# Kernel tuning notes

Hardware: AMD Instinct MI355X
Metric: run time of the kernel (lower is better)

Reference implementation:

```python
import jax, jax.numpy as jnp
import numpy as np

B, C, G, E, R, T, L, K = 8, 192, 256, 384, 4, 8192, 3, 3
DILATIONS = (1, 3, 9)
EPS = 1e-5


def setup_inputs() -> dict:
    key = jax.random.key(0)
    ks = jax.random.split(key, 16)
    s = 0.05
    return {
        'x': jax.random.normal(ks[0], (B, C, T), jnp.float32),
        'x_mask': jnp.ones((B, 1, T), jnp.float32),
        'g': jax.random.normal(ks[1], (B, G, 1), jnp.float32),
        'dconv_w': jax.random.normal(ks[2], (L, C, K), jnp.float32) * s,
        'dconv_b': jax.random.normal(ks[3], (L, C), jnp.float32) * s,
        'ln_gamma': jnp.ones((L, C), jnp.float32),
        'ln_beta': jnp.zeros((L, C), jnp.float32),
        'p1_w': jax.random.normal(ks[4], (L, E, C), jnp.float32) * s,
        'p1_b': jax.random.normal(ks[5], (L, E), jnp.float32) * s,
        'p1_ain_w': jax.random.normal(ks[6], (L, C * R, G), jnp.float32) * 0.01,
        'p1_ain_b': jnp.zeros((L, C * R), jnp.float32),
        'p1_aout_w': jax.random.normal(ks[7], (L, E * R, G), jnp.float32) * 0.01,
        'p1_aout_b': jnp.zeros((L, E * R), jnp.float32),
        'p2_w': jax.random.normal(ks[8], (L, C, E), jnp.float32) * s,
        'p2_b': jax.random.normal(ks[9], (L, C), jnp.float32) * s,
        'p2_ain_w': jax.random.normal(ks[10], (L, E * R, G), jnp.float32) * 0.01,
        'p2_ain_b': jnp.zeros((L, E * R), jnp.float32),
        'p2_aout_w': jax.random.normal(ks[11], (L, C * R, G), jnp.float32) * 0.01,
        'p2_aout_b': jnp.zeros((L, C * R), jnp.float32),
    }


def _causal_dconv(x, w, b, dilation):
    # x: [B,C,T]; w: [C,K] depthwise kernel; matches flip/pad/conv/flip in torch module
    xf = jnp.flip(x, 2)
    xf = jnp.pad(xf, ((0, 0), (0, 0), (0, (K - 1) * dilation)))
    y = jax.lax.conv_general_dilated(
        xf, w[:, None, :], window_strides=(1,), padding='VALID',
        rhs_dilation=(dilation,), dimension_numbers=('NCH', 'OIH', 'NCH'),
        feature_group_count=C)
    y = y + b[None, :, None]
    return jnp.flip(y, 2)


def _layernorm_c(x, gamma, beta):
    # LayerNorm over channel axis (axis=1)
    mu = jnp.mean(x, axis=1, keepdims=True)
    var = jnp.mean(jnp.square(x - mu), axis=1, keepdims=True)
    xn = (x - mu) * jax.lax.rsqrt(var + EPS)
    return xn * gamma[None, :, None] + beta[None, :, None]


def _lora(x, g2, w_main, b_main, ain_w, ain_b, aout_w, aout_b, cin, cout):
    # main 1x1 conv
    x_ = jnp.einsum('oc,bcl->bol', w_main, x) + b_main[None, :, None]
    a_in = (g2 @ ain_w.T + ain_b).reshape(-1, cin, R)      # [B,cin,R]
    a_out = (g2 @ aout_w.T + aout_b).reshape(-1, R, cout)  # [B,R,cout]
    t = jnp.einsum('bcl,bcr->brl', x, a_in)
    low = jnp.einsum('brl,brc->bcl', t, a_out)
    return x_ + low


def reference(x, x_mask, g, dconv_w, dconv_b, ln_gamma, ln_beta,
              p1_w, p1_b, p1_ain_w, p1_ain_b, p1_aout_w, p1_aout_b,
              p2_w, p2_b, p2_ain_w, p2_ain_b, p2_aout_w, p2_aout_b):
    g2 = g[:, :, 0]  # [B,G]
    x = x * x_mask
    for i in range(L):
        residual = x
        h = _causal_dconv(x, dconv_w[i], dconv_b[i], DILATIONS[i])
        h = _layernorm_c(h, ln_gamma[i], ln_beta[i])
        h = h * x_mask
        h = _lora(h, g2, p1_w[i], p1_b[i], p1_ain_w[i], p1_ain_b[i],
                  p1_aout_w[i], p1_aout_b[i], C, E)
        h = jax.nn.gelu(h, approximate=False)
        h = _lora(h, g2, p2_w[i], p2_b[i], p2_ain_w[i], p2_ain_b[i],
                  p2_aout_w[i], p2_aout_b[i], E, C)
        x = residual + h
    return x
```

## Files before the change

kernel.cpp:

```cpp
#include <hip/hip_runtime.h>
#include <hip/hip_bf16.h>

#define B_ 8
#define C_ 192
#define G_ 256
#define E_ 384
#define R_ 4
#define T_ 8192
#define L_ 3
#define K_ 3

typedef __attribute__((ext_vector_type(4))) float f32x4;
typedef __attribute__((ext_vector_type(8))) short bf16x8;
typedef __attribute__((ext_vector_type(4))) short bf16x4;

static __device__ __forceinline__ float bf2f(short u) {
    union { float f; unsigned int i; } z;
    z.i = ((unsigned int)(unsigned short)u) << 16;
    return z.f;
}

static __device__ __forceinline__ float gelu_fast(float x) {
    float e = __expf(-1.702f * x);
    return x / (1.0f + e);
}

__global__ __launch_bounds__(256) void adapters_kernel(
    const float* __restrict__ g2,
    const float* __restrict__ w0, const float* __restrict__ bi0, float* __restrict__ o0,
    const float* __restrict__ w1, const float* __restrict__ bi1, float* __restrict__ o1,
    const float* __restrict__ w2, const float* __restrict__ bi2, float* __restrict__ o2,
    const float* __restrict__ w3, const float* __restrict__ bi3, float* __restrict__ o3)
{
    const int N0 = L_ * B_ * (C_ * R_);
    const int N1 = L_ * B_ * (E_ * R_);
    int idx = blockIdx.x * 256 + threadIdx.x;
    const float* w; const float* bi; float* o; int rows; int li;
    if (idx < N0)                      { w=w0; bi=bi0; o=o0; rows=C_*R_; li=idx; }
    else if ((idx -= N0) < N1)         { w=w1; bi=bi1; o=o1; rows=E_*R_; li=idx; }
    else if ((idx -= N1) < N1)         { w=w2; bi=bi2; o=o2; rows=E_*R_; li=idx; }
    else if ((idx -= N1) < N0)         { w=w3; bi=bi3; o=o3; rows=C_*R_; li=idx; }
    else return;
    int bb = li & 7;
    int lr = li >> 3;
    const float4* wr = (const float4*)(w + (size_t)lr * G_);
    const float4* gb = (const float4*)(g2 + (size_t)bb * G_);
    float s = bi[lr];
#pragma unroll 8
    for (int g = 0; g < G_ / 4; ++g) {
        float4 a = gb[g], b = wr[g];
        s = fmaf(a.x, b.x, s); s = fmaf(a.y, b.y, s);
        s = fmaf(a.z, b.z, s); s = fmaf(a.w, b.w, s);
    }
    o[((size_t)(lr / rows) * B_ + bb) * rows + (lr % rows)] = s;
}

__global__ __launch_bounds__(256) void builds_kernel(
    const float* __restrict__ p1w, const float* __restrict__ p2w,
    const float* __restrict__ gam, const float* __restrict__ bet,
    const float* __restrict__ A1in, const float* __restrict__ A1out,
    const float* __restrict__ A2in, const float* __restrict__ A2out,
    __hip_bfloat16* __restrict__ W1, __hip_bfloat16* __restrict__ W2,
    float* __restrict__ C1)
{
    const int W1B = (L_ * B_ * E_ * C_) / 256;
    int blk = blockIdx.x;
    if (blk < W1B) {
        int idx = blk * 256 + threadIdx.x;
        int c = idx % C_;
        int e = (idx / C_) % E_;
        int b = (idx / (C_ * E_)) % B_;
        int l = idx / (C_ * E_ * B_);
        float v = p1w[((size_t)l * E_ + e) * C_ + c];
        const float* ai = A1in + ((size_t)l * B_ + b) * (C_ * R_);
        const float* ao = A1out + ((size_t)l * B_ + b) * (R_ * E_);
#pragma unroll
        for (int r = 0; r < R_; ++r) v = fmaf(ai[c * R_ + r], ao[r * E_ + e], v);
        W1[idx] = __float2bfloat16(v * gam[l * C_ + c]);
    } else if (blk < 2 * W1B) {
        int idx = (blk - W1B) * 256 + threadIdx.x;
        int e = idx % E_;
        int c = (idx / E_) % C_;
        int b = (idx / (C_ * E_)) % B_;
        int l = idx / (C_ * E_ * B_);
        float v = p2w[((size_t)l * C_ + c) * E_ + e];
        const float* ai = A2in + ((size_t)l * B_ + b) * (E_ * R_);
        const float* ao = A2out + ((size_t)l * B_ + b) * (R_ * C_);
#pragma unroll
        for (int r = 0; r < R_; ++r) v = fmaf(ai[e * R_ + r], ao[r * C_ + c], v);
        W2[idx] = __float2bfloat16(v);
    } else {
        int idx = (blk - 2 * W1B) * 256 + threadIdx.x;
        if (idx >= L_ * B_ * E_) return;
        int e = idx % E_;
        int b = (idx / E_) % B_;
        int l = idx / (E_ * B_);
        const float* wrow = p1w + ((size_t)l * E_ + e) * C_;
        const float* ai = A1in + ((size_t)l * B_ + b) * (C_ * R_);
        const float* ao = A1out + ((size_t)l * B_ + b) * (R_ * E_);
        const float* bt = bet + l * C_;
        float s = 0.f;
        for (int c = 0; c < C_; ++c) {
            float v = wrow[c];
#pragma unroll
            for (int r = 0; r < R_; ++r) v = fmaf(ai[c * R_ + r], ao[r * E_ + e], v);
            s = fmaf(v, bt[c], s);
        }
        C1[((size_t)l * B_ + b) * E_ + e] = s;
    }
}

__global__ __launch_bounds__(256) void transpose_in_kernel(
    const float* __restrict__ x, const float* __restrict__ mask,
    __hip_bfloat16* __restrict__ xw)
{
    __shared__ float tile[64][65];
    int b = blockIdx.z, c0 = blockIdx.y * 64, t0 = blockIdx.x * 64;
#pragma unroll
    for (int it = 0; it < 4; ++it) {
        int i = it * 256 + threadIdx.x;
        int r = i >> 4, cq = i & 15;
        float4 xv = *(const float4*)(&x[((size_t)b * C_ + c0 + r) * T_ + t0 + cq * 4]);
        float4 mv = *(const float4*)(&mask[(size_t)b * T_ + t0 + cq * 4]);
        tile[r][cq * 4 + 0] = xv.x * mv.x;
        tile[r][cq * 4 + 1] = xv.y * mv.y;
        tile[r][cq * 4 + 2] = xv.z * mv.z;
        tile[r][cq * 4 + 3] = xv.w * mv.w;
    }
    __syncthreads();
#pragma unroll
    for (int it = 0; it < 4; ++it) {
        int i = it * 256 + threadIdx.x;
        int r = i >> 4, cq = i & 15;
        union { __hip_bfloat16 h[4]; int2 i2; } u;
#pragma unroll
        for (int j = 0; j < 4; ++j) u.h[j] = __float2bfloat16(tile[cq * 4 + j][r]);
        *(int2*)(&xw[((size_t)b * T_ + t0 + r) * C_ + c0 + cq * 4]) = u.i2;
    }
}

__global__ __launch_bounds__(256) void transpose_out_kernel(
    const __hip_bfloat16* __restrict__ xw, float* __restrict__ out)
{
    __shared__ float tile[64][65];
    int b = blockIdx.z, c0 = blockIdx.y * 64, t0 = blockIdx.x * 64;
#pragma unroll
    for (int it = 0; it < 4; ++it) {
        int i = it * 256 + threadIdx.x;
        int r = i >> 4, cq = i & 15;
        bf16x4 v = *(const bf16x4*)(&xw[((size_t)b * T_ + t0 + r) * C_ + c0 + cq * 4]);
#pragma unroll
        for (int j = 0; j < 4; ++j) tile[cq * 4 + j][r] = bf2f(v[j]);
    }
    __syncthreads();
#pragma unroll
    for (int it = 0; it < 4; ++it) {
        int i = it * 256 + threadIdx.x;
        int r = i >> 4, cq = i & 15;
        float4 o;
        o.x = tile[r][cq * 4 + 0];
        o.y = tile[r][cq * 4 + 1];
        o.z = tile[r][cq * 4 + 2];
        o.w = tile[r][cq * 4 + 3];
        *(float4*)(&out[((size_t)b * C_ + c0 + r) * T_ + t0 + cq * 4]) = o;
    }
}

__global__ __launch_bounds__(256, 2) void ffn_fused_kernel(
    const __hip_bfloat16* __restrict__ xin, __hip_bfloat16* __restrict__ xout,
    const float* __restrict__ dw, const float* __restrict__ db,
    const float* __restrict__ mask,
    const __hip_bfloat16* __restrict__ W1, const float* __restrict__ b1,
    const float* __restrict__ c1,
    const __hip_bfloat16* __restrict__ W2, const float* __restrict__ b2,
    int dil)
{
    __shared__ __hip_bfloat16 Hs[64][C_ + 8];
    __shared__ __hip_bfloat16 H1s[64][E_ + 8];
    const int b = blockIdx.y;
    const int t0 = blockIdx.x * 64;
    const int tid = threadIdx.x;
    const int wv = tid >> 6, lane = tid & 63;
    const int llo = lane & 15, lhi = lane >> 4;
    const size_t xbase = (size_t)b * T_ * C_;

    {
        const int grp = tid >> 4, gl = tid & 15;
        const int cbase = gl * 12;
        float4 wf[9], dbf[3];
#pragma unroll
        for (int q = 0; q < 9; ++q) wf[q] = *(const float4*)(dw + cbase * 3 + q * 4);
#pragma unroll
        for (int q = 0; q < 3; ++q) dbf[q] = *(const float4*)(db + cbase + q * 4);
#pragma unroll
        for (int rr = 0; rr < 4; ++rr) {
            int tl = grp * 4 + rr;
            int t = t0 + tl;
            float v[12];
#pragma unroll
            for (int j = 0; j < 12; ++j) v[j] = ((const float*)dbf)[j];
#pragma unroll
            for (int k3 = 0; k3 < 3; ++k3) {
                int tt = t - k3 * dil;
                if (tt >= 0) {
                    const __hip_bfloat16* rp = xin + xbase + (size_t)tt * C_ + cbase;
#pragma unroll
                    for (int q = 0; q < 3; ++q) {
                        bf16x4 xv = *(const bf16x4*)(rp + q * 4);
#pragma unroll
                        for (int jj = 0; jj < 4; ++jj) {
                            int j = q * 4 + jj;
                            v[j] = fmaf(((const float*)wf)[j * 3 + k3], bf2f(xv[jj]), v[j]);
                        }
                    }
                }
            }
            float s = 0.f, sq = 0.f;
#pragma unroll
            for (int j = 0; j < 12; ++j) { s += v[j]; sq = fmaf(v[j], v[j], sq); }
#pragma unroll
            for (int o = 1; o <= 8; o <<= 1) {
                s += __shfl_xor(s, o, 64);
                sq += __shfl_xor(sq, o, 64);
            }
            float mu = s * (1.f / C_);
            float var = fmaf(sq, 1.f / C_, -mu * mu);
            float rs = rsqrtf(var + 1e-5f);
            float m = mask[(size_t)b * T_ + t];
            float sc = rs * m;
            float sh = -mu * sc;
            union { __hip_bfloat16 h[12]; int2 i2[3]; } u;
#pragma unroll
            for (int j = 0; j < 12; ++j)
                u.h[j] = __float2bfloat16(fmaf(v[j], sc, sh));
#pragma unroll
            for (int q = 0; q < 3; ++q)
                *(int2*)(&Hs[tl][cbase + q * 4]) = u.i2[q];
        }
    }
    __syncthreads();

    const __hip_bfloat16* w1p = W1 + (size_t)b * E_ * C_
        + (size_t)(wv * 96 + llo) * C_ + lhi * 8;
    f32x4 acc1[6][4] = {};
    {
        bf16x8 af[6], afn[6], bfr[4], bfrn[4];
#pragma unroll
        for (int mf = 0; mf < 6; ++mf)
            af[mf] = *(const bf16x8*)(w1p + (size_t)mf * 16 * C_);
#pragma unroll
        for (int nf = 0; nf < 4; ++nf)
            bfr[nf] = *(const bf16x8*)(&Hs[nf * 16 + llo][lhi * 8]);
#pragma unroll
        for (int kc = 0; kc < 6; ++kc) {
            if (kc < 5) {
#pragma unroll
                for (int mf = 0; mf < 6; ++mf)
                    afn[mf] = *(const bf16x8*)(w1p + (size_t)mf * 16 * C_ + (kc + 1) * 32);
#pragma unroll
                for (int nf = 0; nf < 4; ++nf)
                    bfrn[nf] = *(const bf16x8*)(&Hs[nf * 16 + llo][(kc + 1) * 32 + lhi * 8]);
            }
#pragma unroll
            for (int mf = 0; mf < 6; ++mf)
#pragma unroll
                for (int nf = 0; nf < 4; ++nf)
                    acc1[mf][nf] = __builtin_amdgcn_mfma_f32_16x16x32_bf16(
                        af[mf], bfr[nf], acc1[mf][nf], 0, 0, 0);
#pragma unroll
            for (int mf = 0; mf < 6; ++mf) af[mf] = afn[mf];
#pragma unroll
            for (int nf = 0; nf < 4; ++nf) bfr[nf] = bfrn[nf];
        }
    }

    float mcol[4];
#pragma unroll
    for (int nf = 0; nf < 4; ++nf)
        mcol[nf] = mask[(size_t)b * T_ + t0 + nf * 16 + llo];
#pragma unroll
    for (int mf = 0; mf < 6; ++mf) {
        int e0 = wv * 96 + mf * 16 + lhi * 4;
        float4 b1v = *(const float4*)(b1 + e0);
        float4 c1v = *(const float4*)(c1 + (size_t)b * E_ + e0);
#pragma unroll
        for (int nf = 0; nf < 4; ++nf) {
            union { __hip_bfloat16 h[4]; int2 i2; } u;
#pragma unroll
            for (int j = 0; j < 4; ++j) {
                float xx = acc1[mf][nf][j] + ((const float*)&b1v)[j]
                         + mcol[nf] * ((const float*)&c1v)[j];
                u.h[j] = __float2bfloat16(gelu_fast(xx));
            }
            *(int2*)(&H1s[nf * 16 + llo][e0]) = u.i2;
        }
    }
    __syncthreads();

    const __hip_bfloat16* w2p = W2 + (size_t)b * C_ * E_
        + (size_t)(wv * 48 + llo) * E_ + lhi * 8;
    f32x4 acc2[3][4] = {};
    {
        bf16x8 af[3], afn[3], bfr[4], bfrn[4];
#pragma unroll
        for (int mf = 0; mf < 3; ++mf)
            af[mf] = *(const bf16x8*)(w2p + (size_t)mf * 16 * E_);
#pragma unroll
        for (int nf = 0; nf < 4; ++nf)
            bfr[nf] = *(const bf16x8*)(&H1s[nf * 16 + llo][lhi * 8]);
#pragma unroll
        for (int kc = 0; kc < 12; ++kc) {
            if (kc < 11) {
#pragma unroll
                for (int mf = 0; mf < 3; ++mf)
                    afn[mf] = *(const bf16x8*)(w2p + (size_t)mf * 16 * E_ + (kc + 1) * 32);
#pragma unroll
                for (int nf = 0; nf < 4; ++nf)
                    bfrn[nf] = *(const bf16x8*)(&H1s[nf * 16 + llo][(kc + 1) * 32 + lhi * 8]);
            }
#pragma unroll
            for (int mf = 0; mf < 3; ++mf)
#pragma unroll
                for (int nf = 0; nf < 4; ++nf)
                    acc2[mf][nf] = __builtin_amdgcn_mfma_f32_16x16x32_bf16(
                        af[mf], bfr[nf], acc2[mf][nf], 0, 0, 0);
#pragma unroll
            for (int mf = 0; mf < 3; ++mf) af[mf] = afn[mf];
#pragma unroll
            for (int nf = 0; nf < 4; ++nf) bfr[nf] = bfrn[nf];
        }
    }

#pragma unroll
    for (int mf = 0; mf < 3; ++mf) {
        int c0 = wv * 48 + mf * 16 + lhi * 4;
        float4 b2v = *(const float4*)(b2 + c0);
#pragma unroll
        for (int nf = 0; nf < 4; ++nf) {
            int t = t0 + nf * 16 + llo;
            const __hip_bfloat16* pr = xin + xbase + (size_t)t * C_ + c0;
            __hip_bfloat16* po = xout + xbase + (size_t)t * C_ + c0;
            union { __hip_bfloat16 h[4]; int2 i2; } ui, uo;
            ui.i2 = *(const int2*)pr;
#pragma unroll
            for (int j = 0; j < 4; ++j)
                uo.h[j] = __float2bfloat16(
                    bf2f(*(short*)&ui.h[j]) + acc2[mf][nf][j] + ((const float*)&b2v)[j]);
            *(int2*)po = uo.i2;
        }
    }
}

extern "C" void kernel_launch(void* const* d_in, const int* in_sizes, int n_in,
                              void* d_out, int out_size, void* d_ws, size_t ws_size,
                              hipStream_t stream) {
    const float* x        = (const float*)d_in[0];
    const float* x_mask   = (const float*)d_in[1];
    const float* g        = (const float*)d_in[2];
    const float* dconv_w  = (const float*)d_in[3];
    const float* dconv_b  = (const float*)d_in[4];
    const float* ln_gamma = (const float*)d_in[5];
    const float* ln_beta  = (const float*)d_in[6];
    const float* p1_w     = (const float*)d_in[7];
    const float* p1_b     = (const float*)d_in[8];
    const float* p1_ain_w = (const float*)d_in[9];
    const float* p1_ain_b = (const float*)d_in[10];
    const float* p1_aout_w= (const float*)d_in[11];
    const float* p1_aout_b= (const float*)d_in[12];
    const float* p2_w     = (const float*)d_in[13];
    const float* p2_b     = (const float*)d_in[14];
    const float* p2_ain_w = (const float*)d_in[15];
    const float* p2_ain_b = (const float*)d_in[16];
    const float* p2_aout_w= (const float*)d_in[17];
    const float* p2_aout_b= (const float*)d_in[18];

    char* ws = (char*)d_ws;
    size_t off = 0;
    __hip_bfloat16* xwA = (__hip_bfloat16*)(ws + off); off += (size_t)B_ * T_ * C_ * 2;
    __hip_bfloat16* xwB = (__hip_bfloat16*)(ws + off); off += (size_t)B_ * T_ * C_ * 2;
    __hip_bfloat16* W1 = (__hip_bfloat16*)(ws + off);  off += (size_t)L_ * B_ * E_ * C_ * 2;
    __hip_bfloat16* W2 = (__hip_bfloat16*)(ws + off);  off += (size_t)L_ * B_ * C_ * E_ * 2;
    float* C1    = (float*)(ws + off); off += (size_t)L_ * B_ * E_ * 4;
    float* A1in  = (float*)(ws + off); off += (size_t)L_ * B_ * C_ * R_ * 4;
    float* A1out = (float*)(ws + off); off += (size_t)L_ * B_ * R_ * E_ * 4;
    float* A2in  = (float*)(ws + off); off += (size_t)L_ * B_ * E_ * R_ * 4;
    float* A2out = (float*)(ws + off); off += (size_t)L_ * B_ * R_ * C_ * 4;

    {
        int total = L_ * B_ * (2 * C_ * R_ + 2 * E_ * R_);
        adapters_kernel<<<(total + 255) / 256, 256, 0, stream>>>(
            g,
            p1_ain_w, p1_ain_b, A1in,
            p1_aout_w, p1_aout_b, A1out,
            p2_ain_w, p2_ain_b, A2in,
            p2_aout_w, p2_aout_b, A2out);
    }
    {
        int w1blocks = (L_ * B_ * E_ * C_) / 256;
        int c1blocks = (L_ * B_ * E_ + 255) / 256;
        builds_kernel<<<2 * w1blocks + c1blocks, 256, 0, stream>>>(
            p1_w, p2_w, ln_gamma, ln_beta,
            A1in, A1out, A2in, A2out, W1, W2, C1);
    }

    transpose_in_kernel<<<dim3(T_ / 64, C_ / 64, B_), 256, 0, stream>>>(x, x_mask, xwA);

    const int DILS[3] = {1, 3, 9};
    __hip_bfloat16* bufs[2] = {xwA, xwB};
    for (int l = 0; l < L_; ++l) {
        ffn_fused_kernel<<<dim3(T_ / 64, B_), 256, 0, stream>>>(
            bufs[l & 1], bufs[(l & 1) ^ 1],
            dconv_w + l * C_ * K_, dconv_b + l * C_, x_mask,
            W1 + (size_t)l * B_ * E_ * C_, p1_b + l * E_,
            C1 + (size_t)l * B_ * E_,
            W2 + (size_t)l * B_ * C_ * E_, p2_b + l * C_, DILS[l]);
    }

    transpose_out_kernel<<<dim3(T_ / 64, C_ / 64, B_), 256, 0, stream>>>(xwB, (float*)d_out);
}
```

Measured before the change: 264.5 us.

## Split fused FFN into two kernels with global H1 in MFMA-fragment layout

```diff
diff --git a/kernel.cpp b/kernel.cpp
--- a/kernel.cpp
+++ b/kernel.cpp
@@ -21,8 +21,13 @@
 }
 
 static __device__ __forceinline__ float gelu_fast(float x) {
-    float e = __expf(-1.702f * x);
-    return x / (1.0f + e);
+    float x2 = x * x;
+    float inner = fmaf(0.044715f * x, x2, x);
+    float e = __expf(1.5957691216057308f * inner);
+    float r = 1.0f / (e + 1.0f);
+    float t = fmaf(-2.0f, r, 1.0f);
+    float s = 0.5f * x;
+    return fmaf(s, t, s);
 }
 
 __global__ __launch_bounds__(256) void adapters_kernel(
@@ -166,21 +171,19 @@
     }
 }
 
-__global__ __launch_bounds__(256, 2) void ffn_fused_kernel(
-    const __hip_bfloat16* __restrict__ xin, __hip_bfloat16* __restrict__ xout,
+
+__global__ __launch_bounds__(512, 2) void stage_gemm1_kernel(
+    const __hip_bfloat16* __restrict__ xin,
     const float* __restrict__ dw, const float* __restrict__ db,
     const float* __restrict__ mask,
     const __hip_bfloat16* __restrict__ W1, const float* __restrict__ b1,
-    const float* __restrict__ c1,
-    const __hip_bfloat16* __restrict__ W2, const float* __restrict__ b2,
-    int dil)
+    const float* __restrict__ c1, __hip_bfloat16* __restrict__ H1, int dil)
 {
     __shared__ __hip_bfloat16 Hs[64][C_ + 8];
-    __shared__ __hip_bfloat16 H1s[64][E_ + 8];
     const int b = blockIdx.y;
     const int t0 = blockIdx.x * 64;
     const int tid = threadIdx.x;
-    const int wv = tid >> 6, lane = tid & 63;
+    const int w = tid >> 6, lane = tid & 63;
     const int llo = lane & 15, lhi = lane >> 4;
     const size_t xbase = (size_t)b * T_ * C_;
 
@@ -193,8 +196,8 @@
 #pragma unroll
         for (int q = 0; q < 3; ++q) dbf[q] = *(const float4*)(db + cbase + q * 4);
 #pragma unroll
-        for (int rr = 0; rr < 4; ++rr) {
-            int tl = grp * 4 + rr;
+        for (int rr = 0; rr < 2; ++rr) {
+            int tl = grp * 2 + rr;
             int t = t0 + tl;
             float v[12];
 #pragma unroll
@@ -241,12 +244,12 @@
     __syncthreads();
 
     const __hip_bfloat16* w1p = W1 + (size_t)b * E_ * C_
-        + (size_t)(wv * 96 + llo) * C_ + lhi * 8;
-    f32x4 acc1[6][4] = {};
+        + (size_t)(w * 48 + llo) * C_ + lhi * 8;
+    f32x4 acc1[3][4] = {};
     {
-        bf16x8 af[6], afn[6], bfr[4], bfrn[4];
-#pragma unroll
-        for (int mf = 0; mf < 6; ++mf)
+        bf16x8 af[3], afn[3], bfr[4], bfrn[4];
+#pragma unroll
+        for (int mf = 0; mf < 3; ++mf)
             af[mf] = *(const bf16x8*)(w1p + (size_t)mf * 16 * C_);
 #pragma unroll
         for (int nf = 0; nf < 4; ++nf)
@@ -255,20 +258,20 @@
         for (int kc = 0; kc < 6; ++kc) {
             if (kc < 5) {
 #pragma unroll
-                for (int mf = 0; mf < 6; ++mf)
+                for (int mf = 0; mf < 3; ++mf)
                     afn[mf] = *(const bf16x8*)(w1p + (size_t)mf * 16 * C_ + (kc + 1) * 32);
 #pragma unroll
                 for (int nf = 0; nf < 4; ++nf)
                     bfrn[nf] = *(const bf16x8*)(&Hs[nf * 16 + llo][(kc + 1) * 32 + lhi * 8]);
             }
 #pragma unroll
-            for (int mf = 0; mf < 6; ++mf)
+            for (int mf = 0; mf < 3; ++mf)
 #pragma unroll
                 for (int nf = 0; nf < 4; ++nf)
                     acc1[mf][nf] = __builtin_amdgcn_mfma_f32_16x16x32_bf16(
                         af[mf], bfr[nf], acc1[mf][nf], 0, 0, 0);
 #pragma unroll
-            for (int mf = 0; mf < 6; ++mf) af[mf] = afn[mf];
+            for (int mf = 0; mf < 3; ++mf) af[mf] = afn[mf];
 #pragma unroll
             for (int nf = 0; nf < 4; ++nf) bfr[nf] = bfrn[nf];
         }
@@ -279,8 +282,10 @@
     for (int nf = 0; nf < 4; ++nf)
         mcol[nf] = mask[(size_t)b * T_ + t0 + nf * 16 + llo];
 #pragma unroll
-    for (int mf = 0; mf < 6; ++mf) {
-        int e0 = wv * 96 + mf * 16 + lhi * 4;
+    for (int mf = 0; mf < 3; ++mf) {
+        int e0 = w * 48 + mf * 16 + lhi * 4;
+        int be = e0 >> 3;
+        int el = e0 & 7;
         float4 b1v = *(const float4*)(b1 + e0);
         float4 c1v = *(const float4*)(c1 + (size_t)b * E_ + e0);
 #pragma unroll
@@ -292,10 +297,24 @@
                          + mcol[nf] * ((const float*)&c1v)[j];
                 u.h[j] = __float2bfloat16(gelu_fast(xx));
             }
-            *(int2*)(&H1s[nf * 16 + llo][e0]) = u.i2;
-        }
-    }
-    __syncthreads();
+            size_t bt = (size_t)(b * 512 + (t0 >> 4) + nf);
+            *(int2*)(&H1[bt * 6144 + be * 128 + llo * 8 + el]) = u.i2;
+        }
+    }
+}
+
+__global__ __launch_bounds__(256, 2) void gemm2_kernel(
+    const __hip_bfloat16* __restrict__ H1,
+    const __hip_bfloat16* __restrict__ W2, const float* __restrict__ b2,
+    const __hip_bfloat16* __restrict__ xin, __hip_bfloat16* __restrict__ xout)
+{
+    const int b = blockIdx.y;
+    const int t0 = blockIdx.x * 64;
+    const int tid = threadIdx.x;
+    const int wv = tid >> 6, lane = tid & 63;
+    const int llo = lane & 15, lhi = lane >> 4;
+    const size_t xbase = (size_t)b * T_ * C_;
+    const __hip_bfloat16* h1b = H1 + (size_t)(b * 512 + (t0 >> 4)) * 6144;
 
     const __hip_bfloat16* w2p = W2 + (size_t)b * C_ * E_
         + (size_t)(wv * 48 + llo) * E_ + lhi * 8;
@@ -307,7 +326,7 @@
             af[mf] = *(const bf16x8*)(w2p + (size_t)mf * 16 * E_);
 #pragma unroll
         for (int nf = 0; nf < 4; ++nf)
-            bfr[nf] = *(const bf16x8*)(&H1s[nf * 16 + llo][lhi * 8]);
+            bfr[nf] = *(const bf16x8*)(h1b + (size_t)nf * 6144 + lhi * 128 + llo * 8);
 #pragma unroll
         for (int kc = 0; kc < 12; ++kc) {
             if (kc < 11) {
@@ -316,7 +335,8 @@
                     afn[mf] = *(const bf16x8*)(w2p + (size_t)mf * 16 * E_ + (kc + 1) * 32);
 #pragma unroll
                 for (int nf = 0; nf < 4; ++nf)
-                    bfrn[nf] = *(const bf16x8*)(&H1s[nf * 16 + llo][(kc + 1) * 32 + lhi * 8]);
+                    bfrn[nf] = *(const bf16x8*)(h1b + (size_t)nf * 6144
+                                                + ((kc + 1) * 4 + lhi) * 128 + llo * 8);
             }
 #pragma unroll
             for (int mf = 0; mf < 3; ++mf)
@@ -386,6 +406,8 @@
     float* A2in  = (float*)(ws + off); off += (size_t)L_ * B_ * E_ * R_ * 4;
     float* A2out = (float*)(ws + off); off += (size_t)L_ * B_ * R_ * C_ * 4;
 
+    __hip_bfloat16* H1 = (__hip_bfloat16*)d_out;
+
     {
         int total = L_ * B_ * (2 * C_ * R_ + 2 * E_ * R_);
         adapters_kernel<<<(total + 255) / 256, 256, 0, stream>>>(
@@ -408,12 +430,14 @@
     const int DILS[3] = {1, 3, 9};
     __hip_bfloat16* bufs[2] = {xwA, xwB};
     for (int l = 0; l < L_; ++l) {
-        ffn_fused_kernel<<<dim3(T_ / 64, B_), 256, 0, stream>>>(
-            bufs[l & 1], bufs[(l & 1) ^ 1],
+        stage_gemm1_kernel<<<dim3(T_ / 64, B_), 512, 0, stream>>>(
+            bufs[l & 1],
             dconv_w + l * C_ * K_, dconv_b + l * C_, x_mask,
             W1 + (size_t)l * B_ * E_ * C_, p1_b + l * E_,
-            C1 + (size_t)l * B_ * E_,
-            W2 + (size_t)l * B_ * C_ * E_, p2_b + l * C_, DILS[l]);
+            C1 + (size_t)l * B_ * E_, H1, DILS[l]);
+        gemm2_kernel<<<dim3(T_ / 64, B_), 256, 0, stream>>>(
+            H1, W2 + (size_t)l * B_ * C_ * E_, p2_b + l * C_,
+            bufs[l & 1], bufs[(l & 1) ^ 1]);
     }
 
     transpose_out_kernel<<<dim3(T_ / 64, C_ / 64, B_), 256, 0, stream>>>(xwB, (float*)d_out);
```

New measurement: 303.5 us. 1.15x slower.
